# Kernel optimization log

Measured on AMD Instinct MI355X. Metric: run time of the kernel, lower is better.

The kernel has to match this reference:

```python
import jax, jax.numpy as jnp
import numpy as np

ALPHA = 0.2          # LeakyReLU slope
COUNTER_COEFF = 0.5  # config.counter_coeff
N = 50000
E = 500000
NFEATS = 256
NHIDS = 256
NHEADS = 8
DH = NHIDS // NHEADS


def _gat_multihead(x_src, x_dst, src, dst, W, b, a_s, a_d, a_b, n_dst):
    """Multi-head GAT: gather-linear-leakyrelu edge attention, segment softmax,
    softmax-weighted scatter sum.  W:[H,F,D] b:[H,D] a_s,a_d:[H,D] a_b:[H].
    Returns [n_dst, H*D] (heads concatenated, as torch.cat over heads)."""
    Wh_s = jnp.einsum('nf,hfd->nhd', x_src, W) + b  # [Ns,H,D]
    Wh_d = jnp.einsum('nf,hfd->nhd', x_dst, W) + b  # [Nd,H,D]
    # a([Wh_src;Wh_dst]) decomposes into src and dst halves of the weight
    es = jnp.einsum('nhd,hd->nh', Wh_s, a_s)
    ed = jnp.einsum('nhd,hd->nh', Wh_d, a_d)
    e = jax.nn.leaky_relu(es[src] + ed[dst] + a_b, ALPHA)  # [E,H]
    # per-destination (mailbox) softmax, numerically stable
    emax = jax.ops.segment_max(e, dst, num_segments=n_dst)
    emax = jnp.where(jnp.isfinite(emax), emax, 0.0)
    ex = jnp.exp(e - emax[dst])
    denom = jax.ops.segment_sum(ex, dst, num_segments=n_dst)
    att = ex / denom[dst]                          # every edge's dst has >=1 edge
    msg = att[:, :, None] * Wh_s[src]              # [E,H,D]
    out = jax.ops.segment_sum(msg, dst, num_segments=n_dst)  # [n_dst,H,D]
    return out.reshape(n_dst, -1)


def _gru_cell(x, h, W_ih, W_hh, b_ih, b_hh):
    gi = x @ W_ih.T + b_ih
    gh = h @ W_hh.T + b_hh
    i_r, i_z, i_n = jnp.split(gi, 3, axis=1)
    h_r, h_z, h_n = jnp.split(gh, 3, axis=1)
    r = jax.nn.sigmoid(i_r + h_r)
    z = jax.nn.sigmoid(i_z + h_z)
    n = jnp.tanh(i_n + r * h_n)
    return (1.0 - z) * n + z * h


def setup_inputs() -> dict:
    key = jax.random.key(0)
    ks = jax.random.split(key, 20)
    xavier = lambda k, shape, fin, fout: jax.random.uniform(
        k, shape, jnp.float32, -1.0, 1.0) * (1.414 * np.sqrt(6.0 / (fin + fout)))
    inp = {}
    inp['h'] = jax.random.normal(ks[0], (N, NFEATS), jnp.float32)
    inp['hp_counter'] = jax.random.normal(ks[1], (N, NHIDS), jnp.float32)
    inp['hp_support'] = jax.random.normal(ks[2], (N, NHIDS), jnp.float32)
    inp['hp_dst'] = jax.random.normal(ks[3], (N, NHIDS), jnp.float32)
    # intra-turn GAT weights (per head)
    inp['W_gat'] = xavier(ks[4], (NHEADS, NFEATS, DH), NFEATS, DH)
    inp['b_gat'] = jnp.zeros((NHEADS, DH), jnp.float32)
    inp['as_gat'] = xavier(ks[5], (NHEADS, DH), 2 * DH, 1)
    inp['ad_gat'] = xavier(ks[6], (NHEADS, DH), 2 * DH, 1)
    inp['ab_gat'] = jnp.zeros((NHEADS,), jnp.float32)
    # cross-turn GAT weights (shared for counter & support: same self.xgat)
    inp['W_x'] = xavier(ks[7], (NHEADS, NHIDS, DH), NHIDS, DH)
    inp['b_x'] = jnp.zeros((NHEADS, DH), jnp.float32)
    inp['as_x'] = xavier(ks[8], (NHEADS, DH), 2 * DH, 1)
    inp['ad_x'] = xavier(ks[9], (NHEADS, DH), 2 * DH, 1)
    inp['ab_x'] = jnp.zeros((NHEADS,), jnp.float32)
    # GRUCell(nhids, nhids)
    s = 1.0 / np.sqrt(NHIDS)
    inp['W_ih'] = jax.random.uniform(ks[10], (3 * NHIDS, NHIDS), jnp.float32, -s, s)
    inp['W_hh'] = jax.random.uniform(ks[11], (3 * NHIDS, NHIDS), jnp.float32, -s, s)
    inp['b_ih'] = jax.random.uniform(ks[12], (3 * NHIDS,), jnp.float32, -s, s)
    inp['b_hh'] = jax.random.uniform(ks[13], (3 * NHIDS,), jnp.float32, -s, s)
    # edge lists
    inp['edge_src'] = jax.random.randint(ks[14], (E,), 0, N, jnp.int32)
    inp['edge_dst'] = jax.random.randint(ks[15], (E,), 0, N, jnp.int32)
    inp['edge_c_src'] = jax.random.randint(ks[16], (E,), 0, N, jnp.int32)
    inp['edge_c_dst'] = jax.random.randint(ks[17], (E,), 0, N, jnp.int32)
    inp['edge_s_src'] = jax.random.randint(ks[18], (E,), 0, N, jnp.int32)
    inp['edge_s_dst'] = jax.random.randint(ks[19], (E,), 0, N, jnp.int32)
    return inp


def reference(h, hp_counter, hp_support, hp_dst,
              W_gat, b_gat, as_gat, ad_gat, ab_gat,
              W_x, b_x, as_x, ad_x, ab_x,
              W_ih, W_hh, b_ih, b_hh,
              edge_src, edge_dst, edge_c_src, edge_c_dst,
              edge_s_src, edge_s_dst):
    # x = self.gat(g, t): intra-turn multi-head GAT on raw features h
    x = _gat_multihead(h, h, edge_src, edge_dst,
                       W_gat, b_gat, as_gat, ad_gat, ab_gat, N)
    # h_c = self.xgat(g, t-1, 'counter'): directed GAT, prev-turn -> current
    h_c = _gat_multihead(hp_counter, hp_dst, edge_c_src, edge_c_dst,
                         W_x, b_x, as_x, ad_x, ab_x, N)
    # h_s = self.xgat(g, t-2, 'support') (same weights)
    h_s = _gat_multihead(hp_support, hp_dst, edge_s_src, edge_s_dst,
                         W_x, b_x, as_x, ad_x, ab_x, N)
    hmix = COUNTER_COEFF * h_c + (1.0 - COUNTER_COEFF) * h_s
    hprime = _gru_cell(x, hmix, W_ih, W_hh, b_ih, b_hh)
    return hprime
```

## Files before the change

kernel.cpp:

```cpp
#include <hip/hip_runtime.h>
#include <math.h>

#define ALPHA 0.2f
#define LOG2E 1.44269504088896f

constexpr int FEATS = 256;
constexpr int HEADS = 8;

typedef unsigned short u16;
typedef __attribute__((ext_vector_type(8))) short bf16x8;
typedef __attribute__((ext_vector_type(4))) float f32x4;

__device__ __forceinline__ u16 f2b(float f) {
    unsigned u = __float_as_uint(f);
    u += 0x7FFF + ((u >> 16) & 1);
    return (u16)(u >> 16);
}
__device__ __forceinline__ float b2f(u16 x) {
    return __uint_as_float(((unsigned)x) << 16);
}
__device__ __forceinline__ unsigned pk2(float lo, float hi) {
    return __builtin_amdgcn_perm(__float_as_uint(hi), __float_as_uint(lo), 0x07060302u);
}
__device__ __forceinline__ void gload16(const void* g, void* l) {
    __builtin_amdgcn_global_load_lds(
        (const __attribute__((address_space(1))) unsigned int*)g,
        (__attribute__((address_space(3))) unsigned int*)l, 16, 0, 0);
}
__device__ __forceinline__ float rsum16(float v) {
    v += __shfl_xor(v, 1); v += __shfl_xor(v, 2);
    v += __shfl_xor(v, 4); v += __shfl_xor(v, 8);
    return v;
}

__global__ __launch_bounds__(512, 4) void proj4_kernel(
    const float* __restrict__ A0, const float* __restrict__ A1,
    const float* __restrict__ A2, const float* __restrict__ A3,
    const u16* __restrict__ Bg, const u16* __restrict__ Bx,
    const float* __restrict__ bg, const float* __restrict__ bx,
    u16* __restrict__ C0, u16* __restrict__ C1,
    u16* __restrict__ C2, u16* __restrict__ C3,
    const float* __restrict__ as_g, const float* __restrict__ ad_g,
    const float* __restrict__ as_x, const float* __restrict__ ad_x,
    float* __restrict__ es1, float* __restrict__ ed1,
    float* __restrict__ esC, float* __restrict__ edD,
    float* __restrict__ esS,
    int M, int NB) {
    __shared__ char As_raw[32768];
    __shared__ char Bs_raw[32768];
    const int tid = threadIdx.x;
    const int lane = tid & 63;
    const int wid = tid >> 6;
    const int wr = wid >> 2, wc = wid & 3;
    const int seg = blockIdx.x / NB;
    const int bm = (blockIdx.x % NB) * 128;
    const int l15 = lane & 15;
    const float* A = (seg == 0) ? A0 : (seg == 1) ? A1 : (seg == 2) ? A2 : A3;
    const u16* B = (seg == 0) ? Bg : Bx;
    const float* bias = (seg == 0) ? bg : bx;
    u16* C = (seg == 0) ? C0 : (seg == 1) ? C1 : (seg == 2) ? C2 : C3;
    const float* asP = (seg == 0) ? as_g : (seg == 2) ? nullptr : as_x;
    const float* adP = (seg == 0) ? ad_g : (seg == 2) ? ad_x : nullptr;
    float* esP = (seg == 0) ? es1 : (seg == 1) ? esC : (seg == 3) ? esS : nullptr;
    float* edP = (seg == 0) ? ed1 : (seg == 2) ? edD : nullptr;

    f32x4 acc[4][4];
#pragma unroll
    for (int m = 0; m < 4; ++m)
#pragma unroll
        for (int n = 0; n < 4; ++n) acc[m][n] = (f32x4)0.f;

    for (int kb = 0; kb < 4; ++kb) {
        const int k0g = kb * 64;
#pragma unroll
        for (int i = 0; i < 4; ++i) {
            int s = i * 512 + tid;
            int row = s >> 4, c16 = s & 15;
            int gr = min(bm + row, M - 1);
            int gcol = k0g + ((c16 ^ (row & 7)) << 2);
            gload16(A + (size_t)gr * 256 + gcol, As_raw + s * 16);
        }
#pragma unroll
        for (int i = 0; i < 4; ++i) {
            int s = i * 512 + tid;
            int row = s >> 3, c16 = s & 7;
            int gcol = k0g + (c16 ^ (row & 7)) * 8;
            gload16(B + (size_t)row * 256 + gcol, Bs_raw + s * 16);
        }
        __syncthreads();
#pragma unroll
        for (int kk = 0; kk < 2; ++kk) {
            const int ko = kk * 32 + (lane >> 4) * 8;
            const int kc = ko >> 3;
            bf16x8 af[4], bfr[4];
#pragma unroll
            for (int m = 0; m < 4; ++m) {
                int row = wr * 64 + m * 16 + l15;
                int r7 = row & 7;
                int u0 = (2 * kc) ^ r7;
                f32x4 lo = *(const f32x4*)(As_raw + row * 256 + u0 * 16);
                f32x4 hi = *(const f32x4*)(As_raw + row * 256 + (u0 ^ 1) * 16);
                union { unsigned u[4]; bf16x8 v; } cv;
                cv.u[0] = pk2(lo.x, lo.y); cv.u[1] = pk2(lo.z, lo.w);
                cv.u[2] = pk2(hi.x, hi.y); cv.u[3] = pk2(hi.z, hi.w);
                af[m] = cv.v;
            }
#pragma unroll
            for (int n = 0; n < 4; ++n) {
                int row = wc * 64 + n * 16 + l15;
                bfr[n] = *(const bf16x8*)(Bs_raw + row * 128 + ((kc ^ (row & 7)) << 4));
            }
#pragma unroll
            for (int m = 0; m < 4; ++m)
#pragma unroll
                for (int n = 0; n < 4; ++n)
                    acc[m][n] = __builtin_amdgcn_mfma_f32_16x16x32_bf16(
                        af[m], bfr[n], acc[m][n], 0, 0, 0);
        }
        __syncthreads();
    }
    const int hb = wc * 2;
    float cS[4], cD[4];
#pragma unroll
    for (int n = 0; n < 4; ++n) {
        int hn = hb + (n >> 1);
        int ix = (n & 1) * 16 + l15;
        cS[n] = asP ? asP[hn * 32 + ix] : 0.f;
        cD[n] = adP ? adP[hn * 32 + ix] : 0.f;
    }
#pragma unroll
    for (int m = 0; m < 4; ++m) {
#pragma unroll
        for (int j = 0; j < 4; ++j) {
            int gr = bm + wr * 64 + m * 16 + (lane >> 4) * 4 + j;
            float tmp[4];
#pragma unroll
            for (int n = 0; n < 4; ++n)
                tmp[n] = acc[m][n][j] + bias[wc * 64 + n * 16 + l15];
            if (gr < M) {
#pragma unroll
                for (int n = 0; n < 4; ++n)
                    C[(size_t)gr * 256 + wc * 64 + n * 16 + l15] = f2b(tmp[n]);
            }
#pragma unroll
            for (int g = 0; g < 2; ++g) {
                if (esP) {
                    float ps = cS[2 * g] * tmp[2 * g] + cS[2 * g + 1] * tmp[2 * g + 1];
                    ps = rsum16(ps);
                    if (l15 == 0 && gr < M) esP[(size_t)gr * 8 + hb + g] = ps * LOG2E;
                }
                if (edP) {
                    float pd = cD[2 * g] * tmp[2 * g] + cD[2 * g + 1] * tmp[2 * g + 1];
                    pd = rsum16(pd);
                    if (l15 == 0 && gr < M) edP[(size_t)gr * 8 + hb + g] = pd * LOG2E;
                }
            }
        }
    }
}

__global__ void prep_kernel(const float* __restrict__ W_gat, const float* __restrict__ W_x,
                            const float* __restrict__ W_ih, const float* __restrict__ W_hh,
                            u16* __restrict__ Bgat, u16* __restrict__ Bx,
                            u16* __restrict__ Bihr, u16* __restrict__ Bhhr) {
    int i = blockIdx.x * 256 + threadIdx.x;
    if (i < 131072) {
        int j = i & 65535;
        int n = j >> 8, f = j & 255;
        int h2 = n >> 5, d = n & 31;
        const float* W = (i < 65536) ? W_gat : W_x;
        u16* Bt = (i < 65536) ? Bgat : Bx;
        Bt[j] = f2b(W[(h2 * 256 + f) * 32 + d]);
    } else {
        int x = i - 131072;
        int lin = (x < 196608) ? x : x - 196608;
        int c = lin >> 8, k = lin & 255;
        int q = c / 48, rr = c - q * 48;
        int g = rr >> 4, jl = rr & 15;
        int orig = (g * 256 + q * 16 + jl) * 256 + k;
        if (x < 196608) Bihr[lin] = f2b(W_ih[orig]);
        else            Bhhr[lin] = f2b(W_hh[orig]);
    }
}

__global__ void count3_kernel(const int* __restrict__ d0, const int* __restrict__ d1,
                              const int* __restrict__ d2, int* __restrict__ cnt,
                              int E, int N) {
    int i = blockIdx.x * blockDim.x + threadIdx.x;
    if (i >= 3 * E) return;
    if (i < E) atomicAdd(&cnt[d0[i]], 1);
    else if (i < 2 * E) atomicAdd(&cnt[N + d1[i - E]], 1);
    else atomicAdd(&cnt[2 * N + d2[i - 2 * E]], 1);
}
__global__ void scan1_kernel(const int* __restrict__ cnt, int* __restrict__ off,
                             int* __restrict__ blksum, int n) {
    __shared__ int tmp[256];
    int t = threadIdx.x;
    int base = blockIdx.x * 1024 + t * 4;
    int v[4];
#pragma unroll
    for (int k = 0; k < 4; ++k) v[k] = (base + k < n) ? cnt[base + k] : 0;
    int s = v[0] + v[1] + v[2] + v[3];
    tmp[t] = s;
    __syncthreads();
    for (int st = 1; st < 256; st <<= 1) {
        int add = (t >= st) ? tmp[t - st] : 0;
        __syncthreads();
        tmp[t] += add;
        __syncthreads();
    }
    int ex = tmp[t] - s;
#pragma unroll
    for (int k = 0; k < 4; ++k) {
        if (base + k < n) off[base + k] = ex;
        ex += v[k];
    }
    if (t == 255) blksum[blockIdx.x] = tmp[255];
}
__global__ void scan2_kernel(int* __restrict__ blksum, int nb) {
    __shared__ int tmp[256];
    int t = threadIdx.x;
    int v = (t < nb) ? blksum[t] : 0;
    tmp[t] = v;
    __syncthreads();
    for (int s = 1; s < 256; s <<= 1) {
        int add = (t >= s) ? tmp[t - s] : 0;
        __syncthreads();
        tmp[t] += add;
        __syncthreads();
    }
    if (t < nb) blksum[t] = tmp[t] - v;
}
__global__ void scan3_kernel(int* __restrict__ off, int* __restrict__ cur,
                             const int* __restrict__ blksum, int n) {
    int i = blockIdx.x * blockDim.x + threadIdx.x;
    if (i < n) {
        int v = off[i] + blksum[i >> 10];
        off[i] = v;
        cur[i] = v;
    }
}
__global__ void fill3_kernel(const int* __restrict__ s0, const int* __restrict__ d0,
                             const int* __restrict__ s1, const int* __restrict__ d1,
                             const int* __restrict__ s2, const int* __restrict__ d2,
                             int* __restrict__ cur, int* __restrict__ srcs, int E, int N) {
    int i = blockIdx.x * blockDim.x + threadIdx.x;
    if (i >= 3 * E) return;
    int s, slot;
    if (i < E) { s = s0[i]; slot = d0[i]; }
    else if (i < 2 * E) { s = s1[i - E]; slot = N + d1[i - E]; }
    else { s = s2[i - 2 * E]; slot = 2 * N + d2[i - 2 * E]; }
    int p = atomicAdd(&cur[slot], 1);
    srcs[p] = s;
}

__device__ __forceinline__ void run_seg(
    const int* __restrict__ srcs, int start, int deg,
    const float* __restrict__ es, const u16* __restrict__ Wh,
    float edv, int o, int hh,
    float& psum, float4& a) {
    psum = 0.f;
    a = make_float4(0.f, 0.f, 0.f, 0.f);
    if (deg <= 0) return;
    int sP = srcs[start];
    int sN = (deg > 1) ? srcs[start + 1] : sP;
    float rawP = es[sP * 8 + hh];
    ushort4 wP = *(const ushort4*)(Wh + (size_t)sP * FEATS + o);
    for (int j = 0; j < deg; ++j) {
        int sNN = (j + 2 < deg) ? srcs[start + j + 2] : sN;
        float rawN = es[sN * 8 + hh];
        ushort4 wN = *(const ushort4*)(Wh + (size_t)sN * FEATS + o);
        float e = rawP + edv;
        e = e > 0.f ? e : ALPHA * e;
        float pe = exp2f(e);
        psum += pe;
        a.x += pe * b2f(wP.x);
        a.y += pe * b2f(wP.y);
        a.z += pe * b2f(wP.z);
        a.w += pe * b2f(wP.w);
        rawP = rawN; wP = wN; sN = sNN;
    }
}

__global__ __launch_bounds__(256) void gather_all_kernel(
    const int* __restrict__ off, const int* __restrict__ cnt,
    const int* __restrict__ srcs,
    const float* __restrict__ es1, const float* __restrict__ ed1,
    const float* __restrict__ esC, const float* __restrict__ edD,
    const float* __restrict__ esS,
    const float* __restrict__ ab_g, const float* __restrict__ ab_x,
    const u16* __restrict__ Wh1, const u16* __restrict__ WhC,
    const u16* __restrict__ WhS3,
    u16* __restrict__ xb, u16* __restrict__ hmixb, int N) {
    int gwid = (blockIdx.x * blockDim.x + threadIdx.x) >> 6;
    if (gwid >= 2 * N) return;
    int lane = threadIdx.x & 63;
    int o = lane * 4, hh = lane >> 3;
    if (gwid < N) {
        int node = gwid;
        float edv = ed1[node * 8 + hh] + ab_g[hh] * LOG2E;
        float psum; float4 a;
        run_seg(srcs, off[node], cnt[node], es1, Wh1, edv, o, hh, psum, a);
        float sc = (cnt[node] > 0) ? (1.0f / psum) : 0.f;
        ushort4 r;
        r.x = f2b(a.x * sc); r.y = f2b(a.y * sc);
        r.z = f2b(a.z * sc); r.w = f2b(a.w * sc);
        *(ushort4*)(xb + (size_t)node * FEATS + o) = r;
    } else {
        int node = gwid - N;
        float edv = edD[node * 8 + hh] + ab_x[hh] * LOG2E;
        float psum2; float4 a2;
        run_seg(srcs, off[N + node], cnt[N + node], esC, WhC, edv, o, hh, psum2, a2);
        float sc2 = (cnt[N + node] > 0) ? (0.5f / psum2) : 0.f;
        float psum3; float4 a3;
        run_seg(srcs, off[2 * N + node], cnt[2 * N + node], esS, WhS3, edv, o, hh, psum3, a3);
        float sc3 = (cnt[2 * N + node] > 0) ? (0.5f / psum3) : 0.f;
        ushort4 r;
        r.x = f2b(a2.x * sc2 + a3.x * sc3);
        r.y = f2b(a2.y * sc2 + a3.y * sc3);
        r.z = f2b(a2.z * sc2 + a3.z * sc3);
        r.w = f2b(a2.w * sc2 + a3.w * sc3);
        *(ushort4*)(hmixb + (size_t)node * FEATS + o) = r;
    }
}

__global__ __launch_bounds__(512, 4) void gru_fused_kernel(
    const u16* __restrict__ xb, const u16* __restrict__ hmixb,
    const u16* __restrict__ Bihr, const u16* __restrict__ Bhhr,
    const float* __restrict__ b_ih, const float* __restrict__ b_hh,
    float* __restrict__ out, int M) {
    __shared__ char As[16384];
    __shared__ char Bs[24576];
    const int tid = threadIdx.x;
    const int lane = tid & 63;
    const int wid = tid >> 6;
    const int wr = wid >> 2, wq = wid & 3;
    const int bt = blockIdx.x;
    const int bm = blockIdx.y * 128;
    const int l15 = lane & 15;

    f32x4 acc[4][3], acc2[4];
#pragma unroll
    for (int m = 0; m < 4; ++m) {
#pragma unroll
        for (int g = 0; g < 3; ++g) acc[m][g] = (f32x4)0.f;
        acc2[m] = (f32x4)0.f;
    }

#pragma unroll
    for (int pass = 0; pass < 2; ++pass) {
        const u16* A = pass ? hmixb : xb;
        const u16* B = pass ? Bhhr : Bihr;
        for (int kb = 0; kb < 4; ++kb) {
            const int k0g = kb * 64;
#pragma unroll
            for (int i = 0; i < 2; ++i) {
                int s = i * 512 + tid;
                int row = s >> 3, c16 = s & 7;
                int gr = min(bm + row, M - 1);
                int gcol = k0g + (c16 ^ (row & 7)) * 8;
                gload16(A + (size_t)gr * 256 + gcol, As + s * 16);
            }
#pragma unroll
            for (int i = 0; i < 3; ++i) {
                int s = i * 512 + tid;
                int row = s >> 3, c16 = s & 7;
                int gcol = k0g + (c16 ^ (row & 7)) * 8;
                gload16(B + (size_t)(bt * 192 + row) * 256 + gcol, Bs + s * 16);
            }
            __syncthreads();
#pragma unroll
            for (int kk = 0; kk < 2; ++kk) {
                const int ko = kk * 32 + (lane >> 4) * 8;
                const int kc = ko >> 3;
                bf16x8 af[4], bfr[3];
#pragma unroll
                for (int m = 0; m < 4; ++m) {
                    int row = wr * 64 + m * 16 + l15;
                    af[m] = *(const bf16x8*)(As + row * 128 + ((kc ^ (row & 7)) << 4));
                }
#pragma unroll
                for (int g = 0; g < 3; ++g) {
                    int row = wq * 48 + g * 16 + l15;
                    bfr[g] = *(const bf16x8*)(Bs + row * 128 + ((kc ^ (row & 7)) << 4));
                }
#pragma unroll
                for (int m = 0; m < 4; ++m) {
#pragma unroll
                    for (int g = 0; g < 3; ++g) {
                        if (pass == 1 && g == 2)
                            acc2[m] = __builtin_amdgcn_mfma_f32_16x16x32_bf16(
                                af[m], bfr[g], acc2[m], 0, 0, 0);
                        else
                            acc[m][g] = __builtin_amdgcn_mfma_f32_16x16x32_bf16(
                                af[m], bfr[g], acc[m][g], 0, 0, 0);
                    }
                }
            }
            __syncthreads();
        }
    }
    const int j = (bt * 4 + wq) * 16 + l15;
    const float bir = b_ih[j], biz = b_ih[256 + j], bin = b_ih[512 + j];
    const float bhr = b_hh[j], bhz = b_hh[256 + j], bhn = b_hh[512 + j];
#pragma unroll
    for (int m = 0; m < 4; ++m) {
#pragma unroll
        for (int jj = 0; jj < 4; ++jj) {
            int row = bm + wr * 64 + m * 16 + (lane >> 4) * 4 + jj;
            if (row < M) {
                float gr_ = acc[m][0][jj] + bir + bhr;
                float gz_ = acc[m][1][jj] + biz + bhz;
                float rr = 1.f / (1.f + exp2f(-gr_ * LOG2E));
                float zz = 1.f / (1.f + exp2f(-gz_ * LOG2E));
                float nn = tanhf(acc[m][2][jj] + bin + rr * (acc2[m][jj] + bhn));
                float hm = b2f(hmixb[(size_t)row * 256 + j]);
                out[(size_t)row * 256 + j] = (1.f - zz) * nn + zz * hm;
            }
        }
    }
}

extern "C" void kernel_launch(void* const* d_in, const int* in_sizes, int n_in,
                              void* d_out, int out_size, void* d_ws, size_t ws_size,
                              hipStream_t stream) {
    const float* h        = (const float*)d_in[0];
    const float* hp_cnt   = (const float*)d_in[1];
    const float* hp_sup   = (const float*)d_in[2];
    const float* hp_dst   = (const float*)d_in[3];
    const float* W_gat    = (const float*)d_in[4];
    const float* b_gat    = (const float*)d_in[5];
    const float* as_gat   = (const float*)d_in[6];
    const float* ad_gat   = (const float*)d_in[7];
    const float* ab_gat   = (const float*)d_in[8];
    const float* W_x      = (const float*)d_in[9];
    const float* b_x      = (const float*)d_in[10];
    const float* as_x     = (const float*)d_in[11];
    const float* ad_x     = (const float*)d_in[12];
    const float* ab_x     = (const float*)d_in[13];
    const float* W_ih     = (const float*)d_in[14];
    const float* W_hh     = (const float*)d_in[15];
    const float* b_ih     = (const float*)d_in[16];
    const float* b_hh     = (const float*)d_in[17];
    const int* e_src      = (const int*)d_in[18];
    const int* e_dst      = (const int*)d_in[19];
    const int* ec_src     = (const int*)d_in[20];
    const int* ec_dst     = (const int*)d_in[21];
    const int* es_src     = (const int*)d_in[22];
    const int* es_dst     = (const int*)d_in[23];

    const int N = in_sizes[0] / FEATS;
    const int E = in_sizes[18];
    const int N8 = N * HEADS;
    const int N3 = 3 * N;
    const int NBLK3 = (N3 + 1023) / 1024;
    const int NB128 = (N + 127) / 128;

    char* ws = (char*)d_ws;
    size_t p = 0;
    u16* Wh1   = (u16*)(ws + p); p += (size_t)N * FEATS * 2;
    u16* WhC   = (u16*)(ws + p); p += (size_t)N * FEATS * 2;
    u16* WhD   = (u16*)(ws + p); p += (size_t)N * FEATS * 2;
    u16* WhS3  = (u16*)(ws + p); p += (size_t)N * FEATS * 2;
    u16* xb    = (u16*)(ws + p); p += (size_t)N * FEATS * 2;
    u16* hmixb = (u16*)(ws + p); p += (size_t)N * FEATS * 2;
    float* es1 = (float*)(ws + p); p += (size_t)N8 * 4;
    float* ed1 = (float*)(ws + p); p += (size_t)N8 * 4;
    float* esC = (float*)(ws + p); p += (size_t)N8 * 4;
    float* edD = (float*)(ws + p); p += (size_t)N8 * 4;
    float* esS = (float*)(ws + p); p += (size_t)N8 * 4;
    int* cnt3  = (int*)(ws + p); p += (size_t)N3 * 4;
    int* off3  = (int*)(ws + p); p += (size_t)N3 * 4;
    int* cur3  = (int*)(ws + p); p += (size_t)N3 * 4;
    int* blks  = (int*)(ws + p); p += 1024;
    int* srcs3 = (int*)(ws + p); p += (size_t)3 * E * 4;
    u16* Bgat  = (u16*)(ws + p); p += 65536 * 2;
    u16* Bx    = (u16*)(ws + p); p += 65536 * 2;
    u16* Bihr  = (u16*)(ws + p); p += 196608 * 2;
    u16* Bhhr  = (u16*)(ws + p); p += 196608 * 2;

    const dim3 blk(256);
    const dim3 blk512(512);
    const int g3E = (3 * E + 255) / 256;

    prep_kernel<<<2048, blk, 0, stream>>>(W_gat, W_x, W_ih, W_hh, Bgat, Bx, Bihr, Bhhr);
    hipMemsetAsync(cnt3, 0, (size_t)N3 * 4, stream);
    count3_kernel<<<g3E, blk, 0, stream>>>(e_dst, ec_dst, es_dst, cnt3, E, N);
    scan1_kernel<<<NBLK3, blk, 0, stream>>>(cnt3, off3, blks, N3);
    scan2_kernel<<<1, blk, 0, stream>>>(blks, NBLK3);
    scan3_kernel<<<(N3 + 255) / 256, blk, 0, stream>>>(off3, cur3, blks, N3);
    fill3_kernel<<<g3E, blk, 0, stream>>>(e_src, e_dst, ec_src, ec_dst, es_src, es_dst,
                                          cur3, srcs3, E, N);

    proj4_kernel<<<4 * NB128, blk512, 0, stream>>>(
        h, hp_cnt, hp_dst, hp_sup, Bgat, Bx, b_gat, b_x,
        Wh1, WhC, WhD, WhS3,
        as_gat, ad_gat, as_x, ad_x,
        es1, ed1, esC, edD, esS, N, NB128);

    gather_all_kernel<<<(2 * N * 64 + 255) / 256, blk, 0, stream>>>(
        off3, cnt3, srcs3, es1, ed1, esC, edD, esS, ab_gat, ab_x,
        Wh1, WhC, WhS3, xb, hmixb, N);

    gru_fused_kernel<<<dim3(4, NB128), blk512, 0, stream>>>(
        xb, hmixb, Bihr, Bhhr, b_ih, b_hh, (float*)d_out, N);
}
```

Before: 497.5 us.

## Merge prep/count and proj/fill launches; interleave counter/support gathers

Folds the weight-conversion kernel and the edge-count kernel into a single launch, and the CSR fill into the projection GEMM launch as extra trailing blocks, cutting launch count and letting the independent work overlap. The cross-GAT gather loop now walks the counter and support edge lists together with software prefetch, so more independent loads are in flight per thread. The mixed GEMM+fill grid puts atomic-heavy blocks next to the LDS-heavy GEMM blocks, and the fill blocks reserve 64KB of static shared memory they never use, which may limit residency.

```diff
diff --git a/kernel.cpp b/kernel.cpp
--- a/kernel.cpp
+++ b/kernel.cpp
@@ -33,7 +33,92 @@
     return v;
 }
 
-__global__ __launch_bounds__(512, 4) void proj4_kernel(
+__global__ void prep_count_kernel(
+    const float* __restrict__ W_gat, const float* __restrict__ W_x,
+    const float* __restrict__ W_ih, const float* __restrict__ W_hh,
+    u16* __restrict__ Bgat, u16* __restrict__ Bx,
+    u16* __restrict__ Bihr, u16* __restrict__ Bhhr,
+    const int* __restrict__ d0, const int* __restrict__ d1,
+    const int* __restrict__ d2, int* __restrict__ cnt, int E, int N) {
+    int b = blockIdx.x;
+    if (b < 2048) {
+        int i = b * 256 + threadIdx.x;
+        if (i < 131072) {
+            int j = i & 65535;
+            int n = j >> 8, f = j & 255;
+            int h2 = n >> 5, d = n & 31;
+            const float* W = (i < 65536) ? W_gat : W_x;
+            u16* Bt = (i < 65536) ? Bgat : Bx;
+            Bt[j] = f2b(W[(h2 * 256 + f) * 32 + d]);
+        } else {
+            int x = i - 131072;
+            int lin = (x < 196608) ? x : x - 196608;
+            int c = lin >> 8, k = lin & 255;
+            int q = c / 48, rr = c - q * 48;
+            int g = rr >> 4, jl = rr & 15;
+            int orig = (g * 256 + q * 16 + jl) * 256 + k;
+            if (x < 196608) Bihr[lin] = f2b(W_ih[orig]);
+            else            Bhhr[lin] = f2b(W_hh[orig]);
+        }
+    } else {
+        int i = (b - 2048) * 256 + threadIdx.x;
+        if (i >= 3 * E) return;
+        if (i < E) atomicAdd(&cnt[d0[i]], 1);
+        else if (i < 2 * E) atomicAdd(&cnt[N + d1[i - E]], 1);
+        else atomicAdd(&cnt[2 * N + d2[i - 2 * E]], 1);
+    }
+}
+
+__global__ void scan1_kernel(const int* __restrict__ cnt, int* __restrict__ off,
+                             int* __restrict__ blksum, int n) {
+    __shared__ int tmp[256];
+    int t = threadIdx.x;
+    int base = blockIdx.x * 1024 + t * 4;
+    int v[4];
+#pragma unroll
+    for (int k = 0; k < 4; ++k) v[k] = (base + k < n) ? cnt[base + k] : 0;
+    int s = v[0] + v[1] + v[2] + v[3];
+    tmp[t] = s;
+    __syncthreads();
+    for (int st = 1; st < 256; st <<= 1) {
+        int add = (t >= st) ? tmp[t - st] : 0;
+        __syncthreads();
+        tmp[t] += add;
+        __syncthreads();
+    }
+    int ex = tmp[t] - s;
+#pragma unroll
+    for (int k = 0; k < 4; ++k) {
+        if (base + k < n) off[base + k] = ex;
+        ex += v[k];
+    }
+    if (t == 255) blksum[blockIdx.x] = tmp[255];
+}
+__global__ void scan2_kernel(int* __restrict__ blksum, int nb) {
+    __shared__ int tmp[256];
+    int t = threadIdx.x;
+    int v = (t < nb) ? blksum[t] : 0;
+    tmp[t] = v;
+    __syncthreads();
+    for (int s = 1; s < 256; s <<= 1) {
+        int add = (t >= s) ? tmp[t - s] : 0;
+        __syncthreads();
+        tmp[t] += add;
+        __syncthreads();
+    }
+    if (t < nb) blksum[t] = tmp[t] - v;
+}
+__global__ void scan3_kernel(int* __restrict__ off, int* __restrict__ cur,
+                             const int* __restrict__ blksum, int n) {
+    int i = blockIdx.x * blockDim.x + threadIdx.x;
+    if (i < n) {
+        int v = off[i] + blksum[i >> 10];
+        off[i] = v;
+        cur[i] = v;
+    }
+}
+
+__global__ __launch_bounds__(512, 4) void projfill_kernel(
     const float* __restrict__ A0, const float* __restrict__ A1,
     const float* __restrict__ A2, const float* __restrict__ A3,
     const u16* __restrict__ Bg, const u16* __restrict__ Bx,
@@ -45,9 +130,25 @@
     float* __restrict__ es1, float* __restrict__ ed1,
     float* __restrict__ esC, float* __restrict__ edD,
     float* __restrict__ esS,
-    int M, int NB) {
+    const int* __restrict__ s0, const int* __restrict__ d0,
+    const int* __restrict__ s1, const int* __restrict__ d1,
+    const int* __restrict__ s2, const int* __restrict__ d2,
+    int* __restrict__ cur, int* __restrict__ srcs,
+    int M, int NB, int E) {
     __shared__ char As_raw[32768];
     __shared__ char Bs_raw[32768];
+    const int P = 4 * NB;
+    if ((int)blockIdx.x >= P) {
+        int i = (blockIdx.x - P) * 512 + threadIdx.x;
+        if (i >= 3 * E) return;
+        int s, slot;
+        if (i < E) { s = s0[i]; slot = d0[i]; }
+        else if (i < 2 * E) { s = s1[i - E]; slot = M + d1[i - E]; }
+        else { s = s2[i - 2 * E]; slot = 2 * M + d2[i - 2 * E]; }
+        int p = atomicAdd(&cur[slot], 1);
+        srcs[p] = s;
+        return;
+    }
     const int tid = threadIdx.x;
     const int lane = tid & 63;
     const int wid = tid >> 6;
@@ -90,8 +191,7 @@
         __syncthreads();
 #pragma unroll
         for (int kk = 0; kk < 2; ++kk) {
-            const int ko = kk * 32 + (lane >> 4) * 8;
-            const int kc = ko >> 3;
+            const int kc = (kk * 32 + (lane >> 4) * 8) >> 3;
             bf16x8 af[4], bfr[4];
 #pragma unroll
             for (int m = 0; m < 4; ++m) {
@@ -157,101 +257,6 @@
             }
         }
     }
-}
-
-__global__ void prep_kernel(const float* __restrict__ W_gat, const float* __restrict__ W_x,
-                            const float* __restrict__ W_ih, const float* __restrict__ W_hh,
-                            u16* __restrict__ Bgat, u16* __restrict__ Bx,
-                            u16* __restrict__ Bihr, u16* __restrict__ Bhhr) {
-    int i = blockIdx.x * 256 + threadIdx.x;
-    if (i < 131072) {
-        int j = i & 65535;
-        int n = j >> 8, f = j & 255;
-        int h2 = n >> 5, d = n & 31;
-        const float* W = (i < 65536) ? W_gat : W_x;
-        u16* Bt = (i < 65536) ? Bgat : Bx;
-        Bt[j] = f2b(W[(h2 * 256 + f) * 32 + d]);
-    } else {
-        int x = i - 131072;
-        int lin = (x < 196608) ? x : x - 196608;
-        int c = lin >> 8, k = lin & 255;
-        int q = c / 48, rr = c - q * 48;
-        int g = rr >> 4, jl = rr & 15;
-        int orig = (g * 256 + q * 16 + jl) * 256 + k;
-        if (x < 196608) Bihr[lin] = f2b(W_ih[orig]);
-        else            Bhhr[lin] = f2b(W_hh[orig]);
-    }
-}
-
-__global__ void count3_kernel(const int* __restrict__ d0, const int* __restrict__ d1,
-                              const int* __restrict__ d2, int* __restrict__ cnt,
-                              int E, int N) {
-    int i = blockIdx.x * blockDim.x + threadIdx.x;
-    if (i >= 3 * E) return;
-    if (i < E) atomicAdd(&cnt[d0[i]], 1);
-    else if (i < 2 * E) atomicAdd(&cnt[N + d1[i - E]], 1);
-    else atomicAdd(&cnt[2 * N + d2[i - 2 * E]], 1);
-}
-__global__ void scan1_kernel(const int* __restrict__ cnt, int* __restrict__ off,
-                             int* __restrict__ blksum, int n) {
-    __shared__ int tmp[256];
-    int t = threadIdx.x;
-    int base = blockIdx.x * 1024 + t * 4;
-    int v[4];
-#pragma unroll
-    for (int k = 0; k < 4; ++k) v[k] = (base + k < n) ? cnt[base + k] : 0;
-    int s = v[0] + v[1] + v[2] + v[3];
-    tmp[t] = s;
-    __syncthreads();
-    for (int st = 1; st < 256; st <<= 1) {
-        int add = (t >= st) ? tmp[t - st] : 0;
-        __syncthreads();
-        tmp[t] += add;
-        __syncthreads();
-    }
-    int ex = tmp[t] - s;
-#pragma unroll
-    for (int k = 0; k < 4; ++k) {
-        if (base + k < n) off[base + k] = ex;
-        ex += v[k];
-    }
-    if (t == 255) blksum[blockIdx.x] = tmp[255];
-}
-__global__ void scan2_kernel(int* __restrict__ blksum, int nb) {
-    __shared__ int tmp[256];
-    int t = threadIdx.x;
-    int v = (t < nb) ? blksum[t] : 0;
-    tmp[t] = v;
-    __syncthreads();
-    for (int s = 1; s < 256; s <<= 1) {
-        int add = (t >= s) ? tmp[t - s] : 0;
-        __syncthreads();
-        tmp[t] += add;
-        __syncthreads();
-    }
-    if (t < nb) blksum[t] = tmp[t] - v;
-}
-__global__ void scan3_kernel(int* __restrict__ off, int* __restrict__ cur,
-                             const int* __restrict__ blksum, int n) {
-    int i = blockIdx.x * blockDim.x + threadIdx.x;
-    if (i < n) {
-        int v = off[i] + blksum[i >> 10];
-        off[i] = v;
-        cur[i] = v;
-    }
-}
-__global__ void fill3_kernel(const int* __restrict__ s0, const int* __restrict__ d0,
-                             const int* __restrict__ s1, const int* __restrict__ d1,
-                             const int* __restrict__ s2, const int* __restrict__ d2,
-                             int* __restrict__ cur, int* __restrict__ srcs, int E, int N) {
-    int i = blockIdx.x * blockDim.x + threadIdx.x;
-    if (i >= 3 * E) return;
-    int s, slot;
-    if (i < E) { s = s0[i]; slot = d0[i]; }
-    else if (i < 2 * E) { s = s1[i - E]; slot = N + d1[i - E]; }
-    else { s = s2[i - 2 * E]; slot = 2 * N + d2[i - 2 * E]; }
-    int p = atomicAdd(&cur[slot], 1);
-    srcs[p] = s;
 }
 
 __device__ __forceinline__ void run_seg(
@@ -309,12 +314,72 @@
     } else {
         int node = gwid - N;
         float edv = edD[node * 8 + hh] + ab_x[hh] * LOG2E;
-        float psum2; float4 a2;
-        run_seg(srcs, off[N + node], cnt[N + node], esC, WhC, edv, o, hh, psum2, a2);
-        float sc2 = (cnt[N + node] > 0) ? (0.5f / psum2) : 0.f;
-        float psum3; float4 a3;
-        run_seg(srcs, off[2 * N + node], cnt[2 * N + node], esS, WhS3, edv, o, hh, psum3, a3);
-        float sc3 = (cnt[2 * N + node] > 0) ? (0.5f / psum3) : 0.f;
+        int st2 = off[N + node],     dg2 = cnt[N + node];
+        int st3 = off[2 * N + node], dg3 = cnt[2 * N + node];
+        float ps2, ps3;
+        float4 a2, a3;
+        if (dg2 > 0 && dg3 > 0) {
+            ps2 = 0.f; ps3 = 0.f;
+            a2 = make_float4(0.f, 0.f, 0.f, 0.f);
+            a3 = make_float4(0.f, 0.f, 0.f, 0.f);
+            int sP2 = srcs[st2];
+            int sN2 = (dg2 > 1) ? srcs[st2 + 1] : sP2;
+            float r2 = esC[sP2 * 8 + hh];
+            ushort4 w2 = *(const ushort4*)(WhC + (size_t)sP2 * FEATS + o);
+            int sP3 = srcs[st3];
+            int sN3 = (dg3 > 1) ? srcs[st3 + 1] : sP3;
+            float r3 = esS[sP3 * 8 + hh];
+            ushort4 w3 = *(const ushort4*)(WhS3 + (size_t)sP3 * FEATS + o);
+            int j2 = 0, j3 = 0;
+            const int c = min(dg2, dg3);
+            for (int t = 0; t < c; ++t) {
+                int sNN2 = (j2 + 2 < dg2) ? srcs[st2 + j2 + 2] : sN2;
+                float rn2 = esC[sN2 * 8 + hh];
+                ushort4 wn2 = *(const ushort4*)(WhC + (size_t)sN2 * FEATS + o);
+                int sNN3 = (j3 + 2 < dg3) ? srcs[st3 + j3 + 2] : sN3;
+                float rn3 = esS[sN3 * 8 + hh];
+                ushort4 wn3 = *(const ushort4*)(WhS3 + (size_t)sN3 * FEATS + o);
+                float e2 = r2 + edv; e2 = e2 > 0.f ? e2 : ALPHA * e2;
+                float p2 = exp2f(e2);
+                ps2 += p2;
+                a2.x += p2 * b2f(w2.x); a2.y += p2 * b2f(w2.y);
+                a2.z += p2 * b2f(w2.z); a2.w += p2 * b2f(w2.w);
+                float e3 = r3 + edv; e3 = e3 > 0.f ? e3 : ALPHA * e3;
+                float p3 = exp2f(e3);
+                ps3 += p3;
+                a3.x += p3 * b2f(w3.x); a3.y += p3 * b2f(w3.y);
+                a3.z += p3 * b2f(w3.z); a3.w += p3 * b2f(w3.w);
+                r2 = rn2; w2 = wn2; sN2 = sNN2; ++j2;
+                r3 = rn3; w3 = wn3; sN3 = sNN3; ++j3;
+            }
+            for (; j2 < dg2; ++j2) {
+                int sNN2 = (j2 + 2 < dg2) ? srcs[st2 + j2 + 2] : sN2;
+                float rn2 = esC[sN2 * 8 + hh];
+                ushort4 wn2 = *(const ushort4*)(WhC + (size_t)sN2 * FEATS + o);
+                float e2 = r2 + edv; e2 = e2 > 0.f ? e2 : ALPHA * e2;
+                float p2 = exp2f(e2);
+                ps2 += p2;
+                a2.x += p2 * b2f(w2.x); a2.y += p2 * b2f(w2.y);
+                a2.z += p2 * b2f(w2.z); a2.w += p2 * b2f(w2.w);
+                r2 = rn2; w2 = wn2; sN2 = sNN2;
+            }
+            for (; j3 < dg3; ++j3) {
+                int sNN3 = (j3 + 2 < dg3) ? srcs[st3 + j3 + 2] : sN3;
+                float rn3 = esS[sN3 * 8 + hh];
+                ushort4 wn3 = *(const ushort4*)(WhS3 + (size_t)sN3 * FEATS + o);
+                float e3 = r3 + edv; e3 = e3 > 0.f ? e3 : ALPHA * e3;
+                float p3 = exp2f(e3);
+                ps3 += p3;
+                a3.x += p3 * b2f(w3.x); a3.y += p3 * b2f(w3.y);
+                a3.z += p3 * b2f(w3.z); a3.w += p3 * b2f(w3.w);
+                r3 = rn3; w3 = wn3; sN3 = sNN3;
+            }
+        } else {
+            run_seg(srcs, st2, dg2, esC, WhC, edv, o, hh, ps2, a2);
+            run_seg(srcs, st3, dg3, esS, WhS3, edv, o, hh, ps3, a3);
+        }
+        float sc2 = (dg2 > 0) ? (0.5f / ps2) : 0.f;
+        float sc3 = (dg3 > 0) ? (0.5f / ps3) : 0.f;
         ushort4 r;
         r.x = f2b(a2.x * sc2 + a3.x * sc3);
         r.y = f2b(a2.y * sc2 + a3.y * sc3);
@@ -371,8 +436,7 @@
             __syncthreads();
 #pragma unroll
             for (int kk = 0; kk < 2; ++kk) {
-                const int ko = kk * 32 + (lane >> 4) * 8;
-                const int kc = ko >> 3;
+                const int kc = (kk * 32 + (lane >> 4) * 8) >> 3;
                 bf16x8 af[4], bfr[3];
 #pragma unroll
                 for (int m = 0; m < 4; ++m) {
@@ -481,22 +545,25 @@
 
     const dim3 blk(256);
     const dim3 blk512(512);
-    const int g3E = (3 * E + 255) / 256;
-
-    prep_kernel<<<2048, blk, 0, stream>>>(W_gat, W_x, W_ih, W_hh, Bgat, Bx, Bihr, Bhhr);
+    const int g3E256 = (3 * E + 255) / 256;
+    const int FILLB = (3 * E + 511) / 512;
+
     hipMemsetAsync(cnt3, 0, (size_t)N3 * 4, stream);
-    count3_kernel<<<g3E, blk, 0, stream>>>(e_dst, ec_dst, es_dst, cnt3, E, N);
+    prep_count_kernel<<<2048 + g3E256, blk, 0, stream>>>(
+        W_gat, W_x, W_ih, W_hh, Bgat, Bx, Bihr, Bhhr,
+        e_dst, ec_dst, es_dst, cnt3, E, N);
+
     scan1_kernel<<<NBLK3, blk, 0, stream>>>(cnt3, off3, blks, N3);
     scan2_kernel<<<1, blk, 0, stream>>>(blks, NBLK3);
     scan3_kernel<<<(N3 + 255) / 256, blk, 0, stream>>>(off3, cur3, blks, N3);
-    fill3_kernel<<<g3E, blk, 0, stream>>>(e_src, e_dst, ec_src, ec_dst, es_src, es_dst,
-                                          cur3, srcs3, E, N);
-
-    proj4_kernel<<<4 * NB128, blk512, 0, stream>>>(
+
+    projfill_kernel<<<4 * NB128 + FILLB, blk512, 0, stream>>>(
         h, hp_cnt, hp_dst, hp_sup, Bgat, Bx, b_gat, b_x,
         Wh1, WhC, WhD, WhS3,
         as_gat, ad_gat, as_x, ad_x,
-        es1, ed1, esC, edD, esS, N, NB128);
+        es1, ed1, esC, edD, esS,
+        e_src, e_dst, ec_src, ec_dst, es_src, es_dst,
+        cur3, srcs3, N, NB128, E);
 
     gather_all_kernel<<<(2 * N * 64 + 255) / 256, blk, 0, stream>>>(
         off3, cnt3, srcs3, es1, ed1, esC, edD, esS, ab_gat, ab_x,
```

Measured after the change: 496.4 us. Within noise of the previous version (-0.2%).
